# Kernel tuning notes

Measured on AMD Instinct MI355X. Metric: run time of the kernel, lower is better.

Reference implementation:

```python
import jax, jax.numpy as jnp
import numpy as np

KS = 3      # kernel size
PAD = 1     # zero padding
STRIDE = 1
N = KS * KS # 9 sampling points per pixel


def _deform_conv(feature, offset, weight):
    """DeformConv2d: bilinear sample at learned offsets then 3x3 conv (no bias)."""
    b, c, h, w = feature.shape
    x = jnp.pad(feature, ((0, 0), (0, 0), (PAD, PAD), (PAD, PAD)))
    hp, wp = h + 2 * PAD, w + 2 * PAD
    dt = feature.dtype
    # p_n: kernel grid offsets, x(rows) first then y(cols) -> (2N,)
    rng = jnp.arange(-(KS - 1) // 2, (KS - 1) // 2 + 1, dtype=dt)
    pn_x, pn_y = jnp.meshgrid(rng, rng, indexing='ij')
    # p_0: base sampling grid starting at 1 (accounts for zero padding)
    p0_x, p0_y = jnp.meshgrid(jnp.arange(1, h + 1, dtype=dt),
                              jnp.arange(1, w + 1, dtype=dt), indexing='ij')
    # sampling locations p = p_0 + p_n + offset, split into x/y -> (b,h,w,N)
    off = jnp.transpose(offset, (0, 2, 3, 1))  # (b,h,w,2N)
    px = p0_x[None, :, :, None] + pn_x.reshape(-1)[None, None, None, :] + off[..., :N]
    py = p0_y[None, :, :, None] + pn_y.reshape(-1)[None, None, None, :] + off[..., N:]
    q_lt_x = jnp.clip(jnp.floor(px), 0, hp - 1)
    q_lt_y = jnp.clip(jnp.floor(py), 0, wp - 1)
    q_rb_x = jnp.clip(jnp.floor(px) + 1, 0, hp - 1)
    q_rb_y = jnp.clip(jnp.floor(py) + 1, 0, wp - 1)
    px = jnp.clip(px, 0, hp - 1)
    py = jnp.clip(py, 0, wp - 1)
    # bilinear weights for the 4 corners
    g_lt = (1 + (q_lt_x - px)) * (1 + (q_lt_y - py))
    g_rb = (1 - (q_rb_x - px)) * (1 - (q_rb_y - py))
    g_lb = (1 + (q_lt_x - px)) * (1 - (q_rb_y - py))
    g_rt = (1 - (q_rb_x - px)) * (1 + (q_lt_y - py))
    x_flat = x.reshape(b, c, hp * wp)

    def gather(qx, qy):
        idx = (qx * wp + qy).astype(jnp.int32).reshape(b, 1, -1)
        v = jnp.take_along_axis(x_flat, jnp.broadcast_to(idx, (b, c, h * w * N)), axis=2)
        return v.reshape(b, c, h, w, N)

    x_off = (g_lt[:, None] * gather(q_lt_x, q_lt_y)
             + g_rb[:, None] * gather(q_rb_x, q_rb_y)
             + g_lb[:, None] * gather(q_lt_x, q_rb_y)
             + g_rt[:, None] * gather(q_rb_x, q_lt_y))  # (b,c,h,w,N)
    # equivalent of _reshape_x_offset + conv(ks, stride=ks)
    x_off = x_off.reshape(b, c, h, w, KS, KS)
    return jnp.einsum('bchwij,ocij->bohw', x_off, weight)


def setup_inputs() -> dict:
    key = jax.random.key(0)
    k1, k2, k3 = jax.random.split(key, 3)
    B, C, H, W = 4, 256, 64, 64
    feature = jax.random.normal(k1, (B, C, H, W), dtype=jnp.float32)
    offset = jax.random.normal(k2, (B, 2 * N, H, W), dtype=jnp.float32)
    weight = jax.random.normal(k3, (C, C, KS, KS), dtype=jnp.float32) / np.sqrt(C * N)
    return {"feature": feature, "offset": offset, "weight": weight}


def reference(feature, offset, weight):
    f1 = jax.nn.relu(_deform_conv(feature, offset, weight))
    return jax.nn.relu(f1 + feature)
```

## Files before the change

kernel.cpp:

```cpp
#include <hip/hip_runtime.h>

#define HW    4096
#define J_TOT 16384
#define K_TOT 2304
#define C_CH  256

typedef unsigned short u16;
typedef unsigned int   u32;
typedef __attribute__((ext_vector_type(8))) short short8;
typedef __attribute__((ext_vector_type(4))) float f32x4;
typedef __attribute__((ext_vector_type(8))) unsigned short us8;

__device__ __forceinline__ float b2f(u16 u) { return __uint_as_float(((u32)u) << 16); }
__device__ __forceinline__ u16 f2b(float x) {
  u32 u = __float_as_uint(x);
  u += 0x7FFFu + ((u >> 16) & 1u);
  return (u16)(u >> 16);
}

__device__ __forceinline__ void gload_lds16(const u16* g, u16* l) {
  __builtin_amdgcn_global_load_lds(
      (__attribute__((address_space(1))) void*)(void*)g,
      (__attribute__((address_space(3))) void*)(void*)l, 16, 0, 0);
}

__global__ void k_detect(const u16* __restrict__ f, int* __restrict__ flag) {
  __shared__ int sh[256];
  int t = threadIdx.x;
  int hits = 0;
  for (int i = t; i < 2048; i += 256) {
    u16 u = f[2 * i];
    int e = (u >> 7) & 0xFF;
    hits += (e >= 100 && e <= 141) ? 1 : 0;
  }
  sh[t] = hits;
  __syncthreads();
  if (t == 0) {
    int s = 0;
    for (int i = 0; i < 256; i++) s += sh[i];
    flag[0] = (s > 1024) ? 1 : 0;
  }
}

__global__ void k_transpose(const void* __restrict__ featv, u16* __restrict__ ftr,
                            const int* __restrict__ flag) {
  __shared__ u16 tile[32][33];
  int isbf = *flag;
  int b = blockIdx.z;
  int hw0 = blockIdx.x << 5;
  int c0 = blockIdx.y << 5;
  int tx = threadIdx.x;
  int ty = threadIdx.y;
  if (isbf) {
    const u16* f = (const u16*)featv;
#pragma unroll
    for (int i = 0; i < 4; i++) {
      int c = c0 + ty + i * 8;
      tile[ty + i * 8][tx] = f[(((size_t)(b * C_CH + c)) << 12) + hw0 + tx];
    }
  } else {
    const float* f = (const float*)featv;
#pragma unroll
    for (int i = 0; i < 4; i++) {
      int c = c0 + ty + i * 8;
      tile[ty + i * 8][tx] = f2b(f[(((size_t)(b * C_CH + c)) << 12) + hw0 + tx]);
    }
  }
  __syncthreads();
#pragma unroll
  for (int i = 0; i < 4; i++) {
    int hw = hw0 + ty + i * 8;
    ftr[(((size_t)(b * HW + hw)) << 8) + c0 + tx] = tile[tx][ty + i * 8];
  }
}

__global__ void k_wconv(const void* __restrict__ wv, u16* __restrict__ Wr,
                        const int* __restrict__ flag) {
  int isbf = *flag;
  int idx = blockIdx.x * 256 + threadIdx.x;
  if (idx >= C_CH * K_TOT) return;
  int c = idx & 255;
  int n = (idx >> 8) % 9;
  int o = idx / K_TOT;
  int src = (o * 256 + c) * 9 + n;
  if (isbf) Wr[idx] = ((const u16*)wv)[src];
  else      Wr[idx] = f2b(((const float*)wv)[src]);
}

__global__ __launch_bounds__(256) void k_gather(const void* __restrict__ offv,
                                                const u16* __restrict__ ftr,
                                                u16* __restrict__ Xt,
                                                const int* __restrict__ flag) {
  __shared__ float gs[9][4][16];
  __shared__ int   isx[9][4][16];
  int isbf = *flag;
  int j0 = blockIdx.x << 4;
  int b = j0 >> 12;
  int hw0 = j0 & (HW - 1);
  int t = threadIdx.x;

  if (t < 144) {
    int p = t & 15, n = t >> 4;
    int hw = hw0 + p;
    int h = hw >> 6, w = hw & 63;
    size_t obi = (((size_t)(b * 18 + n)) << 12) + hw;
    float ox, oy;
    if (isbf) {
      const u16* po = (const u16*)offv;
      ox = b2f(po[obi]);
      oy = b2f(po[obi + (9u << 12)]);
    } else {
      const float* po = (const float*)offv;
      ox = po[obi];
      oy = po[obi + (9u << 12)];
    }
    int ki = n / 3, kj = n % 3;
    float px = (float)(h + ki) + ox;
    float py = (float)(w + kj) + oy;
    float fx = floorf(px), fy = floorf(py);
    float qltx = fminf(fmaxf(fx, 0.f), 65.f);
    float qlty = fminf(fmaxf(fy, 0.f), 65.f);
    float qrbx = fminf(fmaxf(fx + 1.f, 0.f), 65.f);
    float qrby = fminf(fmaxf(fy + 1.f, 0.f), 65.f);
    float pcx = fminf(fmaxf(px, 0.f), 65.f);
    float pcy = fminf(fmaxf(py, 0.f), 65.f);
    float dltx = 1.f + (qltx - pcx);
    float drbx = 1.f - (qrbx - pcx);
    float dlty = 1.f + (qlty - pcy);
    float drby = 1.f - (qrby - pcy);
    float g0 = dltx * dlty;
    float g1 = drbx * drby;
    float g2 = dltx * drby;
    float g3 = drbx * dlty;
    int x0 = (int)qltx, y0 = (int)qlty, x1 = (int)qrbx, y1 = (int)qrby;
    int v0 = (x0 >= 1 && x0 <= 64 && y0 >= 1 && y0 <= 64);
    int v1 = (x1 >= 1 && x1 <= 64 && y1 >= 1 && y1 <= 64);
    int v2 = (x0 >= 1 && x0 <= 64 && y1 >= 1 && y1 <= 64);
    int v3 = (x1 >= 1 && x1 <= 64 && y0 >= 1 && y0 <= 64);
    int base = b << 12;
    isx[n][0][p] = v0 ? ((base + ((x0 - 1) << 6) + (y0 - 1)) << 8) : 0;
    isx[n][1][p] = v1 ? ((base + ((x1 - 1) << 6) + (y1 - 1)) << 8) : 0;
    isx[n][2][p] = v2 ? ((base + ((x0 - 1) << 6) + (y1 - 1)) << 8) : 0;
    isx[n][3][p] = v3 ? ((base + ((x1 - 1) << 6) + (y0 - 1)) << 8) : 0;
    gs[n][0][p] = v0 ? g0 : 0.f;
    gs[n][1][p] = v1 ? g1 : 0.f;
    gs[n][2][p] = v2 ? g2 : 0.f;
    gs[n][3][p] = v3 ? g3 : 0.f;
  }
  __syncthreads();

  int p = t >> 4, cq = t & 15;
  size_t rowb = (size_t)(j0 + p) * K_TOT;
  int cA = cq * 8, cB = 128 + cq * 8;
  for (int n = 0; n < 9; n++) {
    float g0 = gs[n][0][p], g1 = gs[n][1][p], g2 = gs[n][2][p], g3 = gs[n][3][p];
    const u16* f0 = ftr + isx[n][0][p];
    const u16* f1 = ftr + isx[n][1][p];
    const u16* f2 = ftr + isx[n][2][p];
    const u16* f3 = ftr + isx[n][3][p];
    u16* dst = Xt + rowb + n * 256;
#pragma unroll
    for (int half = 0; half < 2; half++) {
      int c = half ? cB : cA;
      us8 r0 = *(const us8*)(f0 + c);
      us8 r1 = *(const us8*)(f1 + c);
      us8 r2 = *(const us8*)(f2 + c);
      us8 r3 = *(const us8*)(f3 + c);
      us8 ov;
#pragma unroll
      for (int i = 0; i < 8; i++) {
        float v = g0 * b2f(r0[i]) + g1 * b2f(r1[i]) + g2 * b2f(r2[i]) + g3 * b2f(r3[i]);
        ov[i] = f2b(v);
      }
      *(us8*)(dst + c) = ov;
    }
  }
}

__global__ __launch_bounds__(256) void k_gemm(const u16* __restrict__ Wr,
                                              const u16* __restrict__ Xt,
                                              const void* __restrict__ featv,
                                              void* __restrict__ outv,
                                              const int* __restrict__ flag) {
  __shared__ u16 Bs[128 * 32];
  __shared__ u16 As[64 * 32];
  int isbf = *flag;
  int jb = blockIdx.x << 7;
  int ob0 = blockIdx.y << 6;
  int t = threadIdx.x;
  int wave = t >> 6, lane = t & 63;
  int wj = wave >> 1, wo = wave & 1;
  int lr = lane & 15, lk = lane >> 4;

  f32x4 acc[2][4];
  f32x4 zero = {0.f, 0.f, 0.f, 0.f};
#pragma unroll
  for (int i = 0; i < 2; i++)
#pragma unroll
    for (int j = 0; j < 4; j++) acc[i][j] = zero;

  int s0 = wave * 64 + lane;
  int s1 = 256 + s0;
  int r0 = s0 >> 2, cg0 = (s0 & 3) ^ ((r0 >> 1) & 3);
  int r1 = s1 >> 2, cg1 = (s1 & 3) ^ ((r1 >> 1) & 3);
  const u16* bg0 = Xt + (size_t)(jb + r0) * K_TOT + cg0 * 8;
  const u16* bg1 = Xt + (size_t)(jb + r1) * K_TOT + cg1 * 8;
  const u16* ag  = Wr + (size_t)(ob0 + r0) * K_TOT + cg0 * 8;
  u16* bl0 = &Bs[wave * 512];
  u16* bl1 = &Bs[2048 + wave * 512];
  u16* al  = &As[wave * 512];

  int swz = (lr >> 1) & 3;
  const u16* ar = &As[(wo * 32 + lr) * 32 + (lk ^ swz) * 8];
  const u16* br = &Bs[(wj * 64 + lr) * 32 + (lk ^ swz) * 8];

  for (int k0 = 0; k0 < K_TOT; k0 += 32) {
    gload_lds16(bg0 + k0, bl0);
    gload_lds16(bg1 + k0, bl1);
    gload_lds16(ag + k0, al);
    __syncthreads();
    short8 a[2], bb[4];
#pragma unroll
    for (int oi = 0; oi < 2; oi++) a[oi] = *(const short8*)(ar + oi * 512);
#pragma unroll
    for (int ji = 0; ji < 4; ji++) bb[ji] = *(const short8*)(br + ji * 512);
#pragma unroll
    for (int oi = 0; oi < 2; oi++)
#pragma unroll
      for (int ji = 0; ji < 4; ji++)
        acc[oi][ji] = __builtin_amdgcn_mfma_f32_16x16x32_bf16(a[oi], bb[ji], acc[oi][ji], 0, 0, 0);
    __syncthreads();
  }

  int lq = lane >> 4;
#pragma unroll
  for (int oi = 0; oi < 2; oi++) {
#pragma unroll
    for (int ji = 0; ji < 4; ji++) {
      int j = jb + wj * 64 + ji * 16 + lr;
      int bb_ = j >> 12, hw = j & (HW - 1);
      int o0 = ob0 + wo * 32 + oi * 16 + lq * 4;
#pragma unroll
      for (int r = 0; r < 4; r++) {
        size_t oidx = (((size_t)(bb_ * C_CH + o0 + r)) << 12) + hw;
        float v = acc[oi][ji][r];
        v = fmaxf(v, 0.f);
        float ft = isbf ? b2f(((const u16*)featv)[oidx]) : ((const float*)featv)[oidx];
        v = fmaxf(v + ft, 0.f);
        if (isbf) ((u16*)outv)[oidx] = f2b(v);
        else      ((float*)outv)[oidx] = v;
      }
    }
  }
}

extern "C" void kernel_launch(void* const* d_in, const int* in_sizes, int n_in,
                              void* d_out, int out_size, void* d_ws, size_t ws_size,
                              hipStream_t stream) {
  const void* feat = d_in[0];
  const void* offs = d_in[1];
  const void* wght = d_in[2];

  const size_t off_flag = 0;
  const size_t off_wr   = 256;
  const size_t off_ftr  = off_wr + (size_t)1179648;
  const size_t off_xt   = off_ftr + (size_t)8388608;
  const size_t need     = off_xt + (size_t)75497472;
  if (ws_size < need) return;

  char* ws = (char*)d_ws;
  int* flag = (int*)(ws + off_flag);
  u16* Wr   = (u16*)(ws + off_wr);
  u16* ftr  = (u16*)(ws + off_ftr);
  u16* Xt   = (u16*)(ws + off_xt);

  k_detect<<<1, 256, 0, stream>>>((const u16*)feat, flag);
  k_transpose<<<dim3(128, 8, 4), dim3(32, 8), 0, stream>>>(feat, ftr, flag);
  k_wconv<<<K_TOT, 256, 0, stream>>>(wght, Wr, flag);
  k_gather<<<J_TOT / 16, 256, 0, stream>>>(offs, ftr, Xt, flag);
  k_gemm<<<dim3(J_TOT / 128, 4), 256, 0, stream>>>(Wr, Xt, feat, d_out, flag);
}
```

Before: 142.3 us.

## Fuse bilinear gather into GEMM, building B tiles in LDS per kernel tap

Merges the gather kernel and the GEMM kernel into one. Each block computes bilinear samples for 64 pixels and one tap directly into an LDS tile, then runs MFMAs against weight fragments loaded straight from global memory. This removes the 75 MB intermediate Xt write and read-back. In exchange, the gather is recomputed once per output-channel half (grid y=2), the A operand is no longer staged through LDS, and each tap's loop has two barriers with gather and MFMA phases serialized.

```diff
diff --git a/kernel.cpp b/kernel.cpp
--- a/kernel.cpp
+++ b/kernel.cpp
@@ -4,6 +4,7 @@
 #define J_TOT 16384
 #define K_TOT 2304
 #define C_CH  256
+#define BROW  264
 
 typedef unsigned short u16;
 typedef unsigned int   u32;
@@ -16,12 +17,6 @@
   u32 u = __float_as_uint(x);
   u += 0x7FFFu + ((u >> 16) & 1u);
   return (u16)(u >> 16);
-}
-
-__device__ __forceinline__ void gload_lds16(const u16* g, u16* l) {
-  __builtin_amdgcn_global_load_lds(
-      (__attribute__((address_space(1))) void*)(void*)g,
-      (__attribute__((address_space(3))) void*)(void*)l, 16, 0, 0);
 }
 
 __global__ void k_detect(const u16* __restrict__ f, int* __restrict__ flag) {
@@ -87,23 +82,38 @@
   else      Wr[idx] = f2b(((const float*)wv)[src]);
 }
 
-__global__ __launch_bounds__(256) void k_gather(const void* __restrict__ offv,
-                                                const u16* __restrict__ ftr,
-                                                u16* __restrict__ Xt,
-                                                const int* __restrict__ flag) {
-  __shared__ float gs[9][4][16];
-  __shared__ int   isx[9][4][16];
+__global__ __launch_bounds__(256, 2) void k_fused(const u16* __restrict__ Wr,
+                                                  const u16* __restrict__ ftr,
+                                                  const void* __restrict__ offv,
+                                                  const void* __restrict__ featv,
+                                                  void* __restrict__ outv,
+                                                  const int* __restrict__ flag) {
+  __shared__ u16 Bs[64 * BROW];
   int isbf = *flag;
-  int j0 = blockIdx.x << 4;
-  int b = j0 >> 12;
-  int hw0 = j0 & (HW - 1);
+  int jb = blockIdx.x << 6;
+  int ob = blockIdx.y << 7;
+  int b  = jb >> 12;
+  int hw0 = jb & (HW - 1);
   int t = threadIdx.x;
-
-  if (t < 144) {
-    int p = t & 15, n = t >> 4;
-    int hw = hw0 + p;
-    int h = hw >> 6, w = hw & 63;
-    size_t obi = (((size_t)(b * 18 + n)) << 12) + hw;
+  int wave = t >> 6, lane = t & 63;
+  int lr = lane & 15, lk = lane >> 4;
+
+  int px = t >> 2, cq = t & 3;
+  int phw = hw0 + px;
+  int ph = phw >> 6, pw = phw & 63;
+
+  const u16* a0 = Wr + (size_t)(ob + wave * 32 + lr) * K_TOT + lk * 8;
+  const u16* a1 = a0 + (size_t)16 * K_TOT;
+
+  f32x4 acc[2][4];
+  f32x4 zero = {0.f, 0.f, 0.f, 0.f};
+#pragma unroll
+  for (int i = 0; i < 2; i++)
+#pragma unroll
+    for (int j = 0; j < 4; j++) acc[i][j] = zero;
+
+  for (int n = 0; n < 9; n++) {
+    size_t obi = (((size_t)(b * 18 + n)) << 12) + phw;
     float ox, oy;
     if (isbf) {
       const u16* po = (const u16*)offv;
@@ -115,15 +125,15 @@
       oy = po[obi + (9u << 12)];
     }
     int ki = n / 3, kj = n % 3;
-    float px = (float)(h + ki) + ox;
-    float py = (float)(w + kj) + oy;
-    float fx = floorf(px), fy = floorf(py);
+    float sx = (float)(ph + ki) + ox;
+    float sy = (float)(pw + kj) + oy;
+    float fx = floorf(sx), fy = floorf(sy);
     float qltx = fminf(fmaxf(fx, 0.f), 65.f);
     float qlty = fminf(fmaxf(fy, 0.f), 65.f);
     float qrbx = fminf(fmaxf(fx + 1.f, 0.f), 65.f);
     float qrby = fminf(fmaxf(fy + 1.f, 0.f), 65.f);
-    float pcx = fminf(fmaxf(px, 0.f), 65.f);
-    float pcy = fminf(fmaxf(py, 0.f), 65.f);
+    float pcx = fminf(fmaxf(sx, 0.f), 65.f);
+    float pcy = fminf(fmaxf(sy, 0.f), 65.f);
     float dltx = 1.f + (qltx - pcx);
     float drbx = 1.f - (qrbx - pcx);
     float dlty = 1.f + (qlty - pcy);
@@ -138,30 +148,23 @@
     int v2 = (x0 >= 1 && x0 <= 64 && y1 >= 1 && y1 <= 64);
     int v3 = (x1 >= 1 && x1 <= 64 && y0 >= 1 && y0 <= 64);
     int base = b << 12;
-    isx[n][0][p] = v0 ? ((base + ((x0 - 1) << 6) + (y0 - 1)) << 8) : 0;
-    isx[n][1][p] = v1 ? ((base + ((x1 - 1) << 6) + (y1 - 1)) << 8) : 0;
-    isx[n][2][p] = v2 ? ((base + ((x0 - 1) << 6) + (y1 - 1)) << 8) : 0;
-    isx[n][3][p] = v3 ? ((base + ((x1 - 1) << 6) + (y0 - 1)) << 8) : 0;
-    gs[n][0][p] = v0 ? g0 : 0.f;
-    gs[n][1][p] = v1 ? g1 : 0.f;
-    gs[n][2][p] = v2 ? g2 : 0.f;
-    gs[n][3][p] = v3 ? g3 : 0.f;
-  }
-  __syncthreads();
-
-  int p = t >> 4, cq = t & 15;
-  size_t rowb = (size_t)(j0 + p) * K_TOT;
-  int cA = cq * 8, cB = 128 + cq * 8;
-  for (int n = 0; n < 9; n++) {
-    float g0 = gs[n][0][p], g1 = gs[n][1][p], g2 = gs[n][2][p], g3 = gs[n][3][p];
-    const u16* f0 = ftr + isx[n][0][p];
-    const u16* f1 = ftr + isx[n][1][p];
-    const u16* f2 = ftr + isx[n][2][p];
-    const u16* f3 = ftr + isx[n][3][p];
-    u16* dst = Xt + rowb + n * 256;
-#pragma unroll
-    for (int half = 0; half < 2; half++) {
-      int c = half ? cB : cA;
+    int i0 = v0 ? ((base + ((x0 - 1) << 6) + (y0 - 1)) << 8) : 0;
+    int i1 = v1 ? ((base + ((x1 - 1) << 6) + (y1 - 1)) << 8) : 0;
+    int i2 = v2 ? ((base + ((x0 - 1) << 6) + (y1 - 1)) << 8) : 0;
+    int i3 = v3 ? ((base + ((x1 - 1) << 6) + (y0 - 1)) << 8) : 0;
+    g0 = v0 ? g0 : 0.f;
+    g1 = v1 ? g1 : 0.f;
+    g2 = v2 ? g2 : 0.f;
+    g3 = v3 ? g3 : 0.f;
+
+    const u16* f0 = ftr + i0;
+    const u16* f1 = ftr + i1;
+    const u16* f2 = ftr + i2;
+    const u16* f3 = ftr + i3;
+    u16* brow = &Bs[px * BROW] + cq * 64;
+#pragma unroll
+    for (int ch = 0; ch < 8; ch++) {
+      int c = cq * 64 + ch * 8;
       us8 r0 = *(const us8*)(f0 + c);
       us8 r1 = *(const us8*)(f1 + c);
       us8 r2 = *(const us8*)(f2 + c);
@@ -172,77 +175,38 @@
         float v = g0 * b2f(r0[i]) + g1 * b2f(r1[i]) + g2 * b2f(r2[i]) + g3 * b2f(r3[i]);
         ov[i] = f2b(v);
       }
-      *(us8*)(dst + c) = ov;
-    }
-  }
-}
-
-__global__ __launch_bounds__(256) void k_gemm(const u16* __restrict__ Wr,
-                                              const u16* __restrict__ Xt,
-                                              const void* __restrict__ featv,
-                                              void* __restrict__ outv,
-                                              const int* __restrict__ flag) {
-  __shared__ u16 Bs[128 * 32];
-  __shared__ u16 As[64 * 32];
-  int isbf = *flag;
-  int jb = blockIdx.x << 7;
-  int ob0 = blockIdx.y << 6;
-  int t = threadIdx.x;
-  int wave = t >> 6, lane = t & 63;
-  int wj = wave >> 1, wo = wave & 1;
-  int lr = lane & 15, lk = lane >> 4;
-
-  f32x4 acc[2][4];
-  f32x4 zero = {0.f, 0.f, 0.f, 0.f};
-#pragma unroll
-  for (int i = 0; i < 2; i++)
-#pragma unroll
-    for (int j = 0; j < 4; j++) acc[i][j] = zero;
-
-  int s0 = wave * 64 + lane;
-  int s1 = 256 + s0;
-  int r0 = s0 >> 2, cg0 = (s0 & 3) ^ ((r0 >> 1) & 3);
-  int r1 = s1 >> 2, cg1 = (s1 & 3) ^ ((r1 >> 1) & 3);
-  const u16* bg0 = Xt + (size_t)(jb + r0) * K_TOT + cg0 * 8;
-  const u16* bg1 = Xt + (size_t)(jb + r1) * K_TOT + cg1 * 8;
-  const u16* ag  = Wr + (size_t)(ob0 + r0) * K_TOT + cg0 * 8;
-  u16* bl0 = &Bs[wave * 512];
-  u16* bl1 = &Bs[2048 + wave * 512];
-  u16* al  = &As[wave * 512];
-
-  int swz = (lr >> 1) & 3;
-  const u16* ar = &As[(wo * 32 + lr) * 32 + (lk ^ swz) * 8];
-  const u16* br = &Bs[(wj * 64 + lr) * 32 + (lk ^ swz) * 8];
-
-  for (int k0 = 0; k0 < K_TOT; k0 += 32) {
-    gload_lds16(bg0 + k0, bl0);
-    gload_lds16(bg1 + k0, bl1);
-    gload_lds16(ag + k0, al);
+      *(us8*)(brow + ch * 8) = ov;
+    }
     __syncthreads();
-    short8 a[2], bb[4];
-#pragma unroll
-    for (int oi = 0; oi < 2; oi++) a[oi] = *(const short8*)(ar + oi * 512);
-#pragma unroll
-    for (int ji = 0; ji < 4; ji++) bb[ji] = *(const short8*)(br + ji * 512);
-#pragma unroll
-    for (int oi = 0; oi < 2; oi++)
+
+    int k0 = n << 8;
+#pragma unroll
+    for (int kc = 0; kc < 8; kc++) {
+      short8 af0 = *(const short8*)(a0 + k0 + kc * 32);
+      short8 af1 = *(const short8*)(a1 + k0 + kc * 32);
+      short8 bf[4];
 #pragma unroll
       for (int ji = 0; ji < 4; ji++)
-        acc[oi][ji] = __builtin_amdgcn_mfma_f32_16x16x32_bf16(a[oi], bb[ji], acc[oi][ji], 0, 0, 0);
+        bf[ji] = *(const short8*)(&Bs[(ji * 16 + lr) * BROW + kc * 32 + lk * 8]);
+#pragma unroll
+      for (int ji = 0; ji < 4; ji++) {
+        acc[0][ji] = __builtin_amdgcn_mfma_f32_16x16x32_bf16(af0, bf[ji], acc[0][ji], 0, 0, 0);
+        acc[1][ji] = __builtin_amdgcn_mfma_f32_16x16x32_bf16(af1, bf[ji], acc[1][ji], 0, 0, 0);
+      }
+    }
     __syncthreads();
   }
 
-  int lq = lane >> 4;
 #pragma unroll
   for (int oi = 0; oi < 2; oi++) {
 #pragma unroll
     for (int ji = 0; ji < 4; ji++) {
-      int j = jb + wj * 64 + ji * 16 + lr;
-      int bb_ = j >> 12, hw = j & (HW - 1);
-      int o0 = ob0 + wo * 32 + oi * 16 + lq * 4;
+      int j = jb + ji * 16 + lr;
+      int hww = j & (HW - 1);
+      int o0 = ob + wave * 32 + oi * 16 + lk * 4;
 #pragma unroll
       for (int r = 0; r < 4; r++) {
-        size_t oidx = (((size_t)(bb_ * C_CH + o0 + r)) << 12) + hw;
+        size_t oidx = (((size_t)(b * C_CH + o0 + r)) << 12) + hww;
         float v = acc[oi][ji][r];
         v = fmaxf(v, 0.f);
         float ft = isbf ? b2f(((const u16*)featv)[oidx]) : ((const float*)featv)[oidx];
@@ -264,19 +228,16 @@
   const size_t off_flag = 0;
   const size_t off_wr   = 256;
   const size_t off_ftr  = off_wr + (size_t)1179648;
-  const size_t off_xt   = off_ftr + (size_t)8388608;
-  const size_t need     = off_xt + (size_t)75497472;
+  const size_t need     = off_ftr + (size_t)8388608;
   if (ws_size < need) return;
 
   char* ws = (char*)d_ws;
   int* flag = (int*)(ws + off_flag);
   u16* Wr   = (u16*)(ws + off_wr);
   u16* ftr  = (u16*)(ws + off_ftr);
-  u16* Xt   = (u16*)(ws + off_xt);
 
   k_detect<<<1, 256, 0, stream>>>((const u16*)feat, flag);
   k_transpose<<<dim3(128, 8, 4), dim3(32, 8), 0, stream>>>(feat, ftr, flag);
   k_wconv<<<K_TOT, 256, 0, stream>>>(wght, Wr, flag);
-  k_gather<<<J_TOT / 16, 256, 0, stream>>>(offs, ftr, Xt, flag);
-  k_gemm<<<dim3(J_TOT / 128, 4), 256, 0, stream>>>(Wr, Xt, feat, d_out, flag);
-}
+  k_fused<<<dim3(J_TOT / 64, 2), 256, 0, stream>>>(Wr, ftr, offs, feat, d_out, flag);
+}
```

Result: slower. 236.0 us (+65.8%).
